# Optimization experiments

Measured on AMD Instinct MI355X. Metric: run time of the kernel, lower is better.

## Reference

```python
import jax, jax.numpy as jnp
import numpy as np

B, T, D, H = 4, 2048, 1024, 16
HD = D // H  # head_dim = 64
SCALE = HD ** -0.5


def setup_inputs() -> dict:
    key = jax.random.key(0)
    k1, k2, k3 = jax.random.split(key, 3)
    x = jax.random.normal(k1, (B, T, D), dtype=jnp.float32)
    # xavier-uniform-like scaling for weights
    qkv_w = jax.random.normal(k2, (3 * D, D), dtype=jnp.float32) * (2.0 / (4 * D)) ** 0.5
    out_w = jax.random.normal(k3, (D, D), dtype=jnp.float32) * (1.0 / D) ** 0.5
    out_b = jnp.zeros((D,), dtype=jnp.float32)
    return {"x": x, "qkv_w": qkv_w, "out_w": out_w, "out_b": out_b}


def reference(x, qkv_w, out_w, out_b):
    Bx, Tx, _ = x.shape
    # qkv projection (nn.Linear: x @ W^T), no bias
    qkv = jnp.einsum('btd,ed->bte', x, qkv_w)  # [B,T,3D]
    qkv = qkv.reshape(Bx, Tx, 3, H, HD).transpose(2, 0, 3, 1, 4)  # [3,B,H,T,hd]
    q, k, v = qkv[0], qkv[1], qkv[2]
    scores = jnp.einsum('bhqd,bhkd->bhqk', q, k) * SCALE  # [B,H,T,T]
    causal = jnp.triu(jnp.ones((Tx, Tx), dtype=bool), k=1)
    scores = jnp.where(causal, -jnp.inf, scores)
    weights = jax.nn.softmax(scores, axis=-1)
    out = jnp.einsum('bhqk,bhkd->bhqd', weights, v)  # [B,H,T,hd]
    out = out.transpose(0, 2, 1, 3).reshape(Bx, Tx, D)
    return jnp.einsum('btd,ed->bte', out, out_w) + out_b
```

## Files before the change

### kernel.cpp

```cpp
#include <hip/hip_runtime.h>
#include <stdint.h>


typedef __bf16 bfx8 __attribute__((ext_vector_type(8)));
typedef float f32x4 __attribute__((ext_vector_type(4)));
typedef float f32x16 __attribute__((ext_vector_type(16)));

__device__ __forceinline__ uint16_t f2b(float f) {
  uint32_t u = __float_as_uint(f);
  u += 0x7fff + ((u >> 16) & 1);
  return (uint16_t)(u >> 16);
}

__device__ __forceinline__ uint32_t cvt_pk(float lo, float hi) {
  uint32_t r;
  asm("v_cvt_pk_bf16_f32 %0, %1, %2" : "=v"(r) : "v"(lo), "v"(hi));
  return r;
}

__device__ __forceinline__ void gld16(const void* g, void* l) {
  __builtin_amdgcn_global_load_lds((const __attribute__((address_space(1))) void*)g,
                                   (__attribute__((address_space(3))) void*)l,
                                   16, 0, 0);
}

__global__ __launch_bounds__(256) void cvt_bf16(const float* __restrict__ in,
                                                uint16_t* __restrict__ out, int n8) {
  int i = blockIdx.x * 256 + threadIdx.x;
  if (i >= n8) return;
  float4 a = ((const float4*)in)[2 * i];
  float4 b = ((const float4*)in)[2 * i + 1];
  union { uint16_t u[8]; uint4 v; } pk;
  pk.u[0] = f2b(a.x); pk.u[1] = f2b(a.y); pk.u[2] = f2b(a.z); pk.u[3] = f2b(a.w);
  pk.u[4] = f2b(b.x); pk.u[5] = f2b(b.y); pk.u[6] = f2b(b.z); pk.u[7] = f2b(b.w);
  ((uint4*)out)[i] = pk.v;
}

template <int OUTF32>
__global__ __launch_bounds__(256) void gemm_bt(const uint16_t* __restrict__ A,
                                               const uint16_t* __restrict__ B,
                                               void* __restrict__ Cout,
                                               const float* __restrict__ bias,
                                               int M, int N, int K, int nbx, int nwg) {
  __shared__ alignas(16) uint16_t As[2][128 * 32];
  __shared__ alignas(16) uint16_t Bs[2][128 * 32];

  int did = blockIdx.x;
  int wg = (did & 7) * (nwg >> 3) + (did >> 3);
  int bx = wg % nbx, by = wg / nbx;
  int m0 = by * 128, n0 = bx * 128;

  int tid = threadIdx.x;
  int lane = tid & 63, wid = tid >> 6;
  int wm = wid >> 1, wn = wid & 1;

  int rs = wid * 16 + (lane >> 2);
  int cs = (lane & 3) * 8;

  f32x4 acc[4][4] = {};

  auto stage = [&](int buf, int kt) {
    int k0 = kt * 32;
    gld16(&A[(size_t)(m0 + rs) * K + k0 + cs],      &As[buf][wid * 512]);
    gld16(&A[(size_t)(m0 + rs + 64) * K + k0 + cs], &As[buf][wid * 512 + 2048]);
    gld16(&B[(size_t)(n0 + rs) * K + k0 + cs],      &Bs[buf][wid * 512]);
    gld16(&B[(size_t)(n0 + rs + 64) * K + k0 + cs], &Bs[buf][wid * 512 + 2048]);
  };

  stage(0, 0);
  __syncthreads();

  int nk = K >> 5;
  int cur = 0;
  int ko = (lane >> 4) * 8;
  for (int kt = 0; kt < nk; ++kt) {
    if (kt + 1 < nk) stage(cur ^ 1, kt + 1);
    bfx8 a[4], b[4];
#pragma unroll
    for (int mi = 0; mi < 4; ++mi)
      a[mi] = *(const bfx8*)&As[cur][(wm * 64 + mi * 16 + (lane & 15)) * 32 + ko];
#pragma unroll
    for (int ni = 0; ni < 4; ++ni)
      b[ni] = *(const bfx8*)&Bs[cur][(wn * 64 + ni * 16 + (lane & 15)) * 32 + ko];
#pragma unroll
    for (int mi = 0; mi < 4; ++mi)
#pragma unroll
      for (int ni = 0; ni < 4; ++ni)
        acc[mi][ni] =
            __builtin_amdgcn_mfma_f32_16x16x32_bf16(a[mi], b[ni], acc[mi][ni], 0, 0, 0);
    __syncthreads();
    cur ^= 1;
  }

#pragma unroll
  for (int mi = 0; mi < 4; ++mi) {
    int row = m0 + wm * 64 + mi * 16 + ((lane >> 4) << 2);
#pragma unroll
    for (int ni = 0; ni < 4; ++ni) {
      int col = n0 + wn * 64 + ni * 16 + (lane & 15);
#pragma unroll
      for (int r = 0; r < 4; ++r) {
        float v = acc[mi][ni][r];
        if (OUTF32)
          ((float*)Cout)[(size_t)(row + r) * N + col] = v + bias[col];
        else
          ((uint16_t*)Cout)[(size_t)(row + r) * N + col] = f2b(v);
      }
    }
  }
}

__global__ __launch_bounds__(256, 4) void flash_attn(const uint16_t* __restrict__ qkv,
                                                     uint16_t* __restrict__ attnb) {
  const int T = 2048, D3 = 3072;
  const float CSC = 0.125f * 1.44269504f;
  __shared__ alignas(16) uint16_t Ks[2][64 * 64];
  __shared__ alignas(16) uint16_t Vt[2][64 * 64];

  int d = blockIdx.x;
  int bh = d & 63;
  int e = d >> 6;
  int hh = e >> 2, aa = e & 3;
  int qb = 4 * hh + ((aa + hh) & 3);
  int b = bh >> 4, h = bh & 15;
  int q0 = qb * 128;

  int tid = threadIdx.x, lane = tid & 63, wid = tid >> 6;
  int l31 = lane & 31, hi = lane >> 5;
  int qw = q0 + wid * 32;
  int swz = (lane & 7) << 3;

  size_t base = (size_t)b * T * D3;
  int hoff = h * 64;
  const uint16_t* kbase = &qkv[base + 1024 + hoff];
  const uint16_t* vbase = &qkv[base + 2048 + hoff];

  bfx8 qf[4];
  {
    const uint16_t* qp = &qkv[base + (size_t)(qw + l31) * D3 + hoff + 8 * hi];
#pragma unroll
    for (int h4 = 0; h4 < 4; ++h4) qf[h4] = *(const bfx8*)(qp + 16 * h4);
  }

  float mC = -1e30f, l_r = 0.f;
  f32x16 acc0 = {}, acc1 = {};

  int ntile = 2 * qb + 2;

  int krow = wid * 16 + (lane >> 3);
  int kc = ((lane & 7) << 3) ^ ((krow & 7) << 3);
  int vr = (tid & 31) * 2;
  int vc = (tid >> 5) * 8;
  uint4 vreg0, vreg1;

  auto loadV = [&](int kv0) {
    vreg0 = *(const uint4*)&vbase[(size_t)(kv0 + vr) * D3 + vc];
    vreg1 = *(const uint4*)&vbase[(size_t)(kv0 + vr + 1) * D3 + vc];
  };
  auto stageK = [&](int buf, int kv0) {
    gld16(&kbase[(size_t)(kv0 + krow) * D3 + kc], &Ks[buf][wid * 1024]);
    gld16(&kbase[(size_t)(kv0 + krow + 8) * D3 + kc], &Ks[buf][wid * 1024 + 512]);
  };
  auto writeV = [&](int buf) {
    union { uint4 v; uint16_t u[8]; } a, c;
    a.v = vreg0; c.v = vreg1;
#pragma unroll
    for (int j = 0; j < 8; ++j) {
      int hd = vc + j;
      uint32_t pk = (uint32_t)a.u[j] | ((uint32_t)c.u[j] << 16);
      *(uint32_t*)&Vt[buf][hd * 64 + (vr ^ ((hd & 7) << 3))] = pk;
    }
  };

  loadV(0);
  stageK(0, 0);
  writeV(0);
  __syncthreads();

  int cur = 0;
  for (int kt = 0; kt < ntile; ++kt) {
    int kv0 = kt << 6;
    bool pre = (kt + 1 < ntile);
    if (pre) { loadV((kt + 1) << 6); stageK(cur ^ 1, (kt + 1) << 6); }

    if (kv0 <= qw) {
      f32x16 st[2] = {};
      __builtin_amdgcn_s_setprio(1);
#pragma unroll
      for (int h4 = 0; h4 < 4; ++h4) {
#pragma unroll
        for (int t = 0; t < 2; ++t) {
          bfx8 kf = *(const bfx8*)&Ks[cur][(32 * t + l31) * 64 + ((16 * h4 + 8 * hi) ^ swz)];
          st[t] = __builtin_amdgcn_mfma_f32_32x32x16_bf16(kf, qf[h4], st[t], 0, 0, 0);
        }
      }
      __builtin_amdgcn_s_setprio(0);

      int q = qw + l31;
      float mloc = -1e30f;
#pragma unroll
      for (int t = 0; t < 2; ++t) {
        int kvt = kv0 + 32 * t;
        bool nm = (kvt + 31 > qw);
#pragma unroll
        for (int r = 0; r < 16; ++r) {
          float v = st[t][r];
          if (nm) {
            int kv = kvt + (r & 3) + 8 * (r >> 2) + 4 * hi;
            if (kv > q) v = -1e30f;
          }
          st[t][r] = v;
          mloc = fmaxf(mloc, v);
        }
      }
      float mS = mloc * CSC;
      mS = fmaxf(mS, __shfl_xor(mS, 32));
      if (!__all(mS - mC <= 8.0f)) {
        float mCn = fmaxf(mC, mS);
        float fac = __builtin_amdgcn_exp2f(mC - mCn);
        mC = mCn;
        l_r *= fac;
        acc0 *= fac;
        acc1 *= fac;
      }
      float lsum = 0.f;
#pragma unroll
      for (int t = 0; t < 2; ++t)
#pragma unroll
        for (int r = 0; r < 16; ++r) {
          float pe = __builtin_amdgcn_exp2f(fmaf(st[t][r], CSC, -mC));
          st[t][r] = pe;
          lsum += pe;
        }
      lsum += __shfl_xor(lsum, 32);
      l_r += lsum;

      int smax = (qw + 31 - kv0) >> 4;
      __builtin_amdgcn_s_setprio(1);
#pragma unroll
      for (int s = 0; s < 4; ++s) {
        if (s <= smax) {
          int t = s >> 1, pb = 8 * (s & 1);
          uint32_t W0 = cvt_pk(st[t][pb + 0], st[t][pb + 1]);
          uint32_t W1 = cvt_pk(st[t][pb + 2], st[t][pb + 3]);
          uint32_t W2 = cvt_pk(st[t][pb + 4], st[t][pb + 5]);
          uint32_t W3 = cvt_pk(st[t][pb + 6], st[t][pb + 7]);
          auto rA = __builtin_amdgcn_permlane32_swap(W0, W2, false, false);
          auto rB = __builtin_amdgcn_permlane32_swap(W1, W3, false, false);
          union { uint32_t u[4]; bfx8 v; } pf;
          pf.u[0] = rA[0]; pf.u[1] = rB[0]; pf.u[2] = rA[1]; pf.u[3] = rB[1];
          bfx8 v0 = *(const bfx8*)&Vt[cur][l31 * 64 + ((16 * s + 8 * hi) ^ swz)];
          acc0 = __builtin_amdgcn_mfma_f32_32x32x16_bf16(v0, pf.v, acc0, 0, 0, 0);
          bfx8 v1 = *(const bfx8*)&Vt[cur][(32 + l31) * 64 + ((16 * s + 8 * hi) ^ swz)];
          acc1 = __builtin_amdgcn_mfma_f32_32x32x16_bf16(v1, pf.v, acc1, 0, 0, 0);
        }
      }
      __builtin_amdgcn_s_setprio(0);
    }

    if (pre) writeV(cur ^ 1);
    __syncthreads();
    cur ^= 1;
  }

  __syncthreads();
  uint16_t* ow = ((uint16_t*)Ks) + wid * 2048;
  float rl = 1.0f / l_r;
#pragma unroll
  for (int f = 0; f < 2; ++f) {
#pragma unroll
    for (int r = 0; r < 16; r += 2) {
      int hd = 32 * f + (r & 3) + 8 * (r >> 2) + 4 * hi;
      float v0 = (f ? acc1[r] : acc0[r]) * rl;
      float v1 = (f ? acc1[r + 1] : acc0[r + 1]) * rl;
      *(uint32_t*)&ow[l31 * 64 + (hd ^ ((l31 & 7) << 3))] = cvt_pk(v0, v1);
    }
  }
  __syncthreads();
  int row = lane >> 1, cb = (lane & 1) * 32;
  int q = q0 + wid * 32 + row;
  int rs = (row & 7) << 3;
  uint16_t* dst = &attnb[(size_t)(b * T + q) * 1024 + hoff + cb];
#pragma unroll
  for (int cc = 0; cc < 4; ++cc)
    *(uint4*)&dst[cc * 8] = *(const uint4*)&ow[row * 64 + ((cb + cc * 8) ^ rs)];
}

extern "C" void kernel_launch(void* const* d_in, const int* in_sizes, int n_in,
                              void* d_out, int out_size, void* d_ws, size_t ws_size,
                              hipStream_t stream) {
  const float* x = (const float*)d_in[0];
  const float* qkv_w = (const float*)d_in[1];
  const float* out_w = (const float*)d_in[2];
  const float* out_b = (const float*)d_in[3];
  float* out = (float*)d_out;

  char* ws = (char*)d_ws;
  uint16_t* xb    = (uint16_t*)(ws);
  uint16_t* qkvb  = (uint16_t*)(ws + 16777216);
  uint16_t* attnb = (uint16_t*)(ws + 67108864);
  uint16_t* wqkvb = (uint16_t*)(ws + 83886080);
  uint16_t* wob   = (uint16_t*)(ws + 90177536);

  cvt_bf16<<<4096, 256, 0, stream>>>(x, xb, 1048576);
  cvt_bf16<<<1536, 256, 0, stream>>>(qkv_w, wqkvb, 393216);
  cvt_bf16<<<512, 256, 0, stream>>>(out_w, wob, 131072);

  gemm_bt<0><<<1536, 256, 0, stream>>>(xb, wqkvb, (void*)qkvb, nullptr,
                                       8192, 3072, 1024, 24, 1536);
  flash_attn<<<1024, 256, 0, stream>>>(qkvb, attnb);
  gemm_bt<1><<<512, 256, 0, stream>>>(attnb, wob, (void*)out, out_b,
                                      8192, 1024, 1024, 8, 512);
}
```

Baseline: 221.3 us.

## Software-pipeline PV MFMA one tile behind QK with triple-buffered V

Restructures the flash-attention loop so the P·V MFMAs of the previous tile run after the current tile's QK^T MFMAs, overlapping the softmax exp work with matrix ops. V is triple-buffered in LDS to keep the deferred tile's data alive. The change also skips the second QK half on diagonal tiles, specialises the causal masking, and defers the cross-half row-sum shuffle to the end. It costs more LDS and registers (the P fragments are held across iterations), and occupancy is lowered from 4 to 3 blocks per SIMD in launch bounds.

```diff
diff --git a/kernel.cpp b/kernel.cpp
--- a/kernel.cpp
+++ b/kernel.cpp
@@ -110,12 +110,12 @@
   }
 }
 
-__global__ __launch_bounds__(256, 4) void flash_attn(const uint16_t* __restrict__ qkv,
+__global__ __launch_bounds__(256, 3) void flash_attn(const uint16_t* __restrict__ qkv,
                                                      uint16_t* __restrict__ attnb) {
   const int T = 2048, D3 = 3072;
   const float CSC = 0.125f * 1.44269504f;
   __shared__ alignas(16) uint16_t Ks[2][64 * 64];
-  __shared__ alignas(16) uint16_t Vt[2][64 * 64];
+  __shared__ alignas(16) uint16_t Vt[3][64 * 64];
 
   int d = blockIdx.x;
   int bh = d & 63;
@@ -144,6 +144,9 @@
 
   float mC = -1e30f, l_r = 0.f;
   f32x16 acc0 = {}, acc1 = {};
+  bfx8 pf[4];
+  int smax_prev = -1;
+  int vb_prev = 0;
 
   int ntile = 2 * qb + 2;
 
@@ -161,15 +164,29 @@
     gld16(&kbase[(size_t)(kv0 + krow) * D3 + kc], &Ks[buf][wid * 1024]);
     gld16(&kbase[(size_t)(kv0 + krow + 8) * D3 + kc], &Ks[buf][wid * 1024 + 512]);
   };
-  auto writeV = [&](int buf) {
+  auto writeV = [&](int vb) {
     union { uint4 v; uint16_t u[8]; } a, c;
     a.v = vreg0; c.v = vreg1;
 #pragma unroll
     for (int j = 0; j < 8; ++j) {
       int hd = vc + j;
       uint32_t pk = (uint32_t)a.u[j] | ((uint32_t)c.u[j] << 16);
-      *(uint32_t*)&Vt[buf][hd * 64 + (vr ^ ((hd & 7) << 3))] = pk;
-    }
+      *(uint32_t*)&Vt[vb][hd * 64 + (vr ^ ((hd & 7) << 3))] = pk;
+    }
+  };
+  auto doPV = [&](int vb, int smx) {
+    const uint16_t* vp = &Vt[vb][0];
+    __builtin_amdgcn_s_setprio(1);
+#pragma unroll
+    for (int s = 0; s < 4; ++s) {
+      if (s <= smx) {
+        bfx8 v0 = *(const bfx8*)&vp[l31 * 64 + ((16 * s + 8 * hi) ^ swz)];
+        acc0 = __builtin_amdgcn_mfma_f32_32x32x16_bf16(v0, pf[s], acc0, 0, 0, 0);
+        bfx8 v1 = *(const bfx8*)&vp[(32 + l31) * 64 + ((16 * s + 8 * hi) ^ swz)];
+        acc1 = __builtin_amdgcn_mfma_f32_32x32x16_bf16(v1, pf[s], acc1, 0, 0, 0);
+      }
+    }
+    __builtin_amdgcn_s_setprio(0);
   };
 
   loadV(0);
@@ -177,95 +194,138 @@
   writeV(0);
   __syncthreads();
 
-  int cur = 0;
   for (int kt = 0; kt < ntile; ++kt) {
     int kv0 = kt << 6;
     bool pre = (kt + 1 < ntile);
-    if (pre) { loadV((kt + 1) << 6); stageK(cur ^ 1, (kt + 1) << 6); }
-
-    if (kv0 <= qw) {
-      f32x16 st[2] = {};
+    if (pre) { loadV((kt + 1) << 6); stageK((kt + 1) & 1, (kt + 1) << 6); }
+
+    int curK = kt & 1;
+    bool active = (kv0 <= qw);
+    int tmax = (qw > kv0) ? 2 : 1;
+    f32x16 st0 = {}, st1 = {};
+
+    if (active) {
       __builtin_amdgcn_s_setprio(1);
 #pragma unroll
       for (int h4 = 0; h4 < 4; ++h4) {
-#pragma unroll
-        for (int t = 0; t < 2; ++t) {
-          bfx8 kf = *(const bfx8*)&Ks[cur][(32 * t + l31) * 64 + ((16 * h4 + 8 * hi) ^ swz)];
-          st[t] = __builtin_amdgcn_mfma_f32_32x32x16_bf16(kf, qf[h4], st[t], 0, 0, 0);
+        bfx8 kf0 = *(const bfx8*)&Ks[curK][l31 * 64 + ((16 * h4 + 8 * hi) ^ swz)];
+        st0 = __builtin_amdgcn_mfma_f32_32x32x16_bf16(kf0, qf[h4], st0, 0, 0, 0);
+        if (tmax == 2) {
+          bfx8 kf1 = *(const bfx8*)&Ks[curK][(32 + l31) * 64 + ((16 * h4 + 8 * hi) ^ swz)];
+          st1 = __builtin_amdgcn_mfma_f32_32x32x16_bf16(kf1, qf[h4], st1, 0, 0, 0);
         }
       }
       __builtin_amdgcn_s_setprio(0);
-
+    }
+
+    if (smax_prev >= 0) {
+      doPV(vb_prev, smax_prev);
+      smax_prev = -1;
+    }
+
+    if (active) {
       int q = qw + l31;
-      float mloc = -1e30f;
-#pragma unroll
-      for (int t = 0; t < 2; ++t) {
-        int kvt = kv0 + 32 * t;
-        bool nm = (kvt + 31 > qw);
+      float mx0 = -1e30f, mx1 = -1e30f;
+      if (kv0 == qw) {
 #pragma unroll
         for (int r = 0; r < 16; ++r) {
-          float v = st[t][r];
-          if (nm) {
-            int kv = kvt + (r & 3) + 8 * (r >> 2) + 4 * hi;
+          int kv = kv0 + (r & 3) + 8 * (r >> 2) + 4 * hi;
+          float v = st0[r];
+          if (kv > q) v = -1e30f;
+          st0[r] = v;
+          mx0 = fmaxf(mx0, v);
+        }
+      } else {
+#pragma unroll
+        for (int r = 0; r < 16; ++r) mx0 = fmaxf(mx0, st0[r]);
+      }
+      if (tmax == 2) {
+        if (kv0 + 32 == qw) {
+#pragma unroll
+          for (int r = 0; r < 16; ++r) {
+            int kv = kv0 + 32 + (r & 3) + 8 * (r >> 2) + 4 * hi;
+            float v = st1[r];
             if (kv > q) v = -1e30f;
+            st1[r] = v;
+            mx1 = fmaxf(mx1, v);
           }
-          st[t][r] = v;
-          mloc = fmaxf(mloc, v);
-        }
-      }
-      float mS = mloc * CSC;
-      mS = fmaxf(mS, __shfl_xor(mS, 32));
+        } else {
+#pragma unroll
+          for (int r = 0; r < 16; ++r) mx1 = fmaxf(mx1, st1[r]);
+        }
+      }
+      float mS = fmaxf(mx0, mx1) * CSC;
       if (!__all(mS - mC <= 8.0f)) {
-        float mCn = fmaxf(mC, mS);
+        float mSp = fmaxf(mS, __shfl_xor(mS, 32));
+        float mCn = fmaxf(mC, mSp);
         float fac = __builtin_amdgcn_exp2f(mC - mCn);
         mC = mCn;
         l_r *= fac;
         acc0 *= fac;
         acc1 *= fac;
       }
-      float lsum = 0.f;
-#pragma unroll
-      for (int t = 0; t < 2; ++t)
-#pragma unroll
-        for (int r = 0; r < 16; ++r) {
-          float pe = __builtin_amdgcn_exp2f(fmaf(st[t][r], CSC, -mC));
-          st[t][r] = pe;
-          lsum += pe;
-        }
-      lsum += __shfl_xor(lsum, 32);
-      l_r += lsum;
+      float l0 = 0.f, l1 = 0.f, l2 = 0.f, l3 = 0.f;
+#pragma unroll
+      for (int r = 0; r < 16; r += 4) {
+        float e0 = __builtin_amdgcn_exp2f(fmaf(st0[r], CSC, -mC));
+        float e1 = __builtin_amdgcn_exp2f(fmaf(st0[r + 1], CSC, -mC));
+        float e2 = __builtin_amdgcn_exp2f(fmaf(st0[r + 2], CSC, -mC));
+        float e3 = __builtin_amdgcn_exp2f(fmaf(st0[r + 3], CSC, -mC));
+        st0[r] = e0; st0[r + 1] = e1; st0[r + 2] = e2; st0[r + 3] = e3;
+        l0 += e0; l1 += e1; l2 += e2; l3 += e3;
+      }
+      if (tmax == 2) {
+#pragma unroll
+        for (int r = 0; r < 16; r += 4) {
+          float e0 = __builtin_amdgcn_exp2f(fmaf(st1[r], CSC, -mC));
+          float e1 = __builtin_amdgcn_exp2f(fmaf(st1[r + 1], CSC, -mC));
+          float e2 = __builtin_amdgcn_exp2f(fmaf(st1[r + 2], CSC, -mC));
+          float e3 = __builtin_amdgcn_exp2f(fmaf(st1[r + 3], CSC, -mC));
+          st1[r] = e0; st1[r + 1] = e1; st1[r + 2] = e2; st1[r + 3] = e3;
+          l0 += e0; l1 += e1; l2 += e2; l3 += e3;
+        }
+      }
+      l_r += (l0 + l1) + (l2 + l3);
 
       int smax = (qw + 31 - kv0) >> 4;
-      __builtin_amdgcn_s_setprio(1);
+      if (smax > 3) smax = 3;
 #pragma unroll
       for (int s = 0; s < 4; ++s) {
         if (s <= smax) {
-          int t = s >> 1, pb = 8 * (s & 1);
-          uint32_t W0 = cvt_pk(st[t][pb + 0], st[t][pb + 1]);
-          uint32_t W1 = cvt_pk(st[t][pb + 2], st[t][pb + 3]);
-          uint32_t W2 = cvt_pk(st[t][pb + 4], st[t][pb + 5]);
-          uint32_t W3 = cvt_pk(st[t][pb + 6], st[t][pb + 7]);
+          int pb = 8 * (s & 1);
+          uint32_t W0, W1, W2, W3;
+          if (s < 2) {
+            W0 = cvt_pk(st0[pb + 0], st0[pb + 1]);
+            W1 = cvt_pk(st0[pb + 2], st0[pb + 3]);
+            W2 = cvt_pk(st0[pb + 4], st0[pb + 5]);
+            W3 = cvt_pk(st0[pb + 6], st0[pb + 7]);
+          } else {
+            W0 = cvt_pk(st1[pb + 0], st1[pb + 1]);
+            W1 = cvt_pk(st1[pb + 2], st1[pb + 3]);
+            W2 = cvt_pk(st1[pb + 4], st1[pb + 5]);
+            W3 = cvt_pk(st1[pb + 6], st1[pb + 7]);
+          }
           auto rA = __builtin_amdgcn_permlane32_swap(W0, W2, false, false);
           auto rB = __builtin_amdgcn_permlane32_swap(W1, W3, false, false);
-          union { uint32_t u[4]; bfx8 v; } pf;
-          pf.u[0] = rA[0]; pf.u[1] = rB[0]; pf.u[2] = rA[1]; pf.u[3] = rB[1];
-          bfx8 v0 = *(const bfx8*)&Vt[cur][l31 * 64 + ((16 * s + 8 * hi) ^ swz)];
-          acc0 = __builtin_amdgcn_mfma_f32_32x32x16_bf16(v0, pf.v, acc0, 0, 0, 0);
-          bfx8 v1 = *(const bfx8*)&Vt[cur][(32 + l31) * 64 + ((16 * s + 8 * hi) ^ swz)];
-          acc1 = __builtin_amdgcn_mfma_f32_32x32x16_bf16(v1, pf.v, acc1, 0, 0, 0);
-        }
-      }
-      __builtin_amdgcn_s_setprio(0);
-    }
-
-    if (pre) writeV(cur ^ 1);
+          union { uint32_t u[4]; bfx8 v; } pk;
+          pk.u[0] = rA[0]; pk.u[1] = rB[0]; pk.u[2] = rA[1]; pk.u[3] = rB[1];
+          pf[s] = pk.v;
+        }
+      }
+      smax_prev = smax;
+      vb_prev = kt % 3;
+    }
+
+    if (pre) writeV((kt + 1) % 3);
     __syncthreads();
-    cur ^= 1;
-  }
-
+  }
+
+  if (smax_prev >= 0) doPV(vb_prev, smax_prev);
+
+  float l_tot = l_r + __shfl_xor(l_r, 32);
   __syncthreads();
   uint16_t* ow = ((uint16_t*)Ks) + wid * 2048;
-  float rl = 1.0f / l_r;
+  float rl = 1.0f / l_tot;
 #pragma unroll
   for (int f = 0; f < 2; ++f) {
 #pragma unroll
```

Result: faster. 197.3 us (-10.8%).
